# Kernel optimization log

Hardware: AMD Instinct MI355X
Metric: run time of the kernel (lower is better)

Reference implementation:

```python
import jax, jax.numpy as jnp
import numpy as np

B, N, NUM = 16384, 512, 3  # batch, num queries, num vanishing points per image


def setup_inputs() -> dict:
    key = jax.random.key(0)
    k1, k2, k3 = jax.random.split(key, 3)
    pred_logits = jax.random.normal(k1, (B, N, 1), jnp.float32)
    pp = jax.random.normal(k2, (B, N, 3), jnp.float32)
    pred_pos = pp / jnp.linalg.norm(pp, axis=-1, keepdims=True)  # unit directions
    vp = jax.random.normal(k3, (B, 3, NUM), jnp.float32)
    vps_unique = vp / jnp.linalg.norm(vp, axis=1, keepdims=True)  # all columns valid (abs-sum > 1e-5)
    return {"pred_logits": pred_logits, "pred_pos": pred_pos, "vps_unique": vps_unique}


def _greedy_select(conf, pos, num):
    # conf: [N,1], pos: [N,3]; greedy angular NMS keeping `num` candidates.
    order = jnp.argsort(-conf[:, 0]).astype(jnp.int32)  # descending confidence
    thresh = jnp.pi / (num + 1)
    ar = jnp.arange(num)
    cand0 = jnp.zeros((num,), jnp.int32).at[0].set(order[0])

    def step(carry, idx):
        cand, count = carry
        sel = pos[cand]                                   # [num,3]
        dots = jnp.minimum(jnp.abs(sel @ pos[idx]), 1.0)  # clip for arccos stability
        ang = jnp.where(ar < count, jnp.arccos(dots), jnp.inf)
        add = (count < num) & (jnp.min(ang) >= thresh)    # torch: skip if dst < pi/(num+1)
        cand = jnp.where(add & (ar == count), idx, cand)
        return (cand, count + add.astype(jnp.int32)), None

    (cand, _), _ = jax.lax.scan(step, (cand0, jnp.int32(1)), order[1:])
    return pos[cand]  # [num,3]


def reference(pred_logits, pred_pos, vps_unique):
    num = vps_unique.shape[2]  # static: all vps columns are valid by construction
    sel = jax.vmap(lambda c, p: _greedy_select(c, p, num))(pred_logits, pred_pos)
    return sel  # [B, num, 3]
```

## Files before the change

kernel.cpp:

```cpp
#include <hip/hip_runtime.h>
#include <math.h>

#define B_TOTAL 16384
#define NQ 512
#define NUM 3

__global__ __launch_bounds__(256) void greedy_nms_kernel(
    const float* __restrict__ conf,
    const float* __restrict__ pos,
    float* __restrict__ out)
{
    const int wave = threadIdx.x >> 6;
    const int lane = threadIdx.x & 63;
    const int b = (blockIdx.x << 2) + wave;

    const float* cb = conf + (size_t)b * NQ;
    const float* pb = pos  + (size_t)b * NQ * 3;

    const float4* cb4 = reinterpret_cast<const float4*>(cb);
    float4 c0 = cb4[lane * 2 + 0];
    float4 c1 = cb4[lane * 2 + 1];
    const float4* pb4 = reinterpret_cast<const float4*>(pb);
    float4 q0 = pb4[lane * 6 + 0];
    float4 q1 = pb4[lane * 6 + 1];
    float4 q2 = pb4[lane * 6 + 2];
    float4 q3 = pb4[lane * 6 + 3];
    float4 q4 = pb4[lane * 6 + 4];
    float4 q5 = pb4[lane * 6 + 5];

    unsigned k[8];
    {
        float f[8] = {c0.x, c0.y, c0.z, c0.w, c1.x, c1.y, c1.z, c1.w};
        #pragma unroll
        for (int s = 0; s < 8; ++s) {
            int bi = __float_as_int(f[s]);
            k[s] = (unsigned)bi ^ ((unsigned)(bi >> 31) | 0x80000000u);
        }
    }

    float rx[8], ry[8], rz[8];
    {
        float fl[24] = {q0.x, q0.y, q0.z, q0.w, q1.x, q1.y, q1.z, q1.w,
                        q2.x, q2.y, q2.z, q2.w, q3.x, q3.y, q3.z, q3.w,
                        q4.x, q4.y, q4.z, q4.w, q5.x, q5.y, q5.z, q5.w};
        #pragma unroll
        for (int j = 0; j < 8; ++j) {
            rx[j] = fl[3 * j + 0];
            ry[j] = fl[3 * j + 1];
            rz[j] = fl[3 * j + 2];
        }
    }

    auto argmax_idx = [&](unsigned& gm_out) -> int {
        unsigned m = k[0];
        #pragma unroll
        for (int s = 1; s < 8; ++s) m = k[s] > m ? k[s] : m;
        unsigned gm = m;
        #pragma unroll
        for (int off = 1; off < 64; off <<= 1) {
            unsigned o = __shfl_xor(gm, off);
            gm = o > gm ? o : gm;
        }
        int sl = 8;
        #pragma unroll
        for (int s = 7; s >= 0; --s)
            if (k[s] == gm) sl = s;
        unsigned long long ball = __ballot(sl < 8);
        int owner = __ffsll(ball) - 1;
        int osl = __shfl(sl, owner);
        gm_out = gm;
        return owner * 8 + osl;
    };

    auto get_row = [&](int w, float& x, float& y, float& z) {
        const int ow = w >> 3, sl = w & 7;
        float tx = rx[0], ty = ry[0], tz = rz[0];
        #pragma unroll
        for (int s = 1; s < 8; ++s)
            if (sl == s) { tx = rx[s]; ty = ry[s]; tz = rz[s]; }
        x = __shfl(tx, ow); y = __shfl(ty, ow); z = __shfl(tz, ow);
    };

    const float TH  = 0.78539816339744830961f;
    const float CLO = 0.70710478f;
    const float CHI = 0.70710878f;

    auto mask_keys = [&](float px, float py, float pz) {
        #pragma unroll
        for (int s = 0; s < 8; ++s) {
            float d = fabsf(rx[s] * px + ry[s] * py + rz[s] * pz);
            bool pass;
            if (d <= CLO)      pass = true;
            else if (d >= CHI) pass = false;
            else               pass = (acosf(fminf(d, 1.f)) >= TH);
            if (!pass) k[s] = 0u;
        }
    };

    unsigned gm1;
    int w1 = argmax_idx(gm1);
    float p1x, p1y, p1z;
    get_row(w1, p1x, p1y, p1z);
    {
        const int osl = ((w1 >> 3) == lane) ? (w1 & 7) : 8;
        #pragma unroll
        for (int s = 0; s < 8; ++s)
            if (osl == s) k[s] = 0u;
    }

    float p0x, p0y, p0z;
    get_row(0, p0x, p0y, p0z);

    mask_keys(p1x, p1y, p1z);
    unsigned gm2;
    int w2 = argmax_idx(gm2);

    float o2x = p0x, o2y = p0y, o2z = p0z;
    float o3x = p0x, o3y = p0y, o3z = p0z;

    if (gm2 != 0u) {
        float p2x, p2y, p2z;
        get_row(w2, p2x, p2y, p2z);
        o2x = p2x; o2y = p2y; o2z = p2z;

        mask_keys(p2x, p2y, p2z);
        unsigned gm3;
        int w3 = argmax_idx(gm3);
        if (gm3 != 0u) {
            get_row(w3, o3x, o3y, o3z);
        }
    }

    if (lane == 0) {
        float* ob = out + (size_t)b * 9;
        ob[0] = p1x; ob[1] = p1y; ob[2] = p1z;
        ob[3] = o2x; ob[4] = o2y; ob[5] = o2z;
        ob[6] = o3x; ob[7] = o3y; ob[8] = o3z;
    }
}

extern "C" void kernel_launch(void* const* d_in, const int* in_sizes, int n_in,
                              void* d_out, int out_size, void* d_ws, size_t ws_size,
                              hipStream_t stream) {
    const float* pred_logits = (const float*)d_in[0];
    const float* pred_pos    = (const float*)d_in[1];
    float* out = (float*)d_out;

    const int grid = B_TOTAL / 4;
    greedy_nms_kernel<<<grid, 256, 0, stream>>>(pred_logits, pred_pos, out);
}
```

Baseline: 26.64 us.

## Process four batches per wave with double-buffered register prefetch

Cuts the grid to 4096 waves, each handling four images strided across the batch. The loads for the next image are issued into a second register stage before the current one is processed, so memory latency overlaps with the argmax and masking work. This costs higher register pressure from two live stages, which may lower occupancy, and leaves fewer waves to hide latency through the hardware scheduler.

```diff
diff --git a/kernel.cpp b/kernel.cpp
--- a/kernel.cpp
+++ b/kernel.cpp
@@ -4,139 +4,159 @@
 #define B_TOTAL 16384
 #define NQ 512
 #define NUM 3
+#define WAVES_TOTAL 4096
+
+struct Stage {
+    float4 c0, c1;
+    float4 q0, q1, q2, q3, q4, q5;
+};
 
 __global__ __launch_bounds__(256) void greedy_nms_kernel(
     const float* __restrict__ conf,
     const float* __restrict__ pos,
     float* __restrict__ out)
 {
-    const int wave = threadIdx.x >> 6;
     const int lane = threadIdx.x & 63;
-    const int b = (blockIdx.x << 2) + wave;
+    const int wg   = (blockIdx.x << 2) | (threadIdx.x >> 6);
 
-    const float* cb = conf + (size_t)b * NQ;
-    const float* pb = pos  + (size_t)b * NQ * 3;
-
-    const float4* cb4 = reinterpret_cast<const float4*>(cb);
-    float4 c0 = cb4[lane * 2 + 0];
-    float4 c1 = cb4[lane * 2 + 1];
-    const float4* pb4 = reinterpret_cast<const float4*>(pb);
-    float4 q0 = pb4[lane * 6 + 0];
-    float4 q1 = pb4[lane * 6 + 1];
-    float4 q2 = pb4[lane * 6 + 2];
-    float4 q3 = pb4[lane * 6 + 3];
-    float4 q4 = pb4[lane * 6 + 4];
-    float4 q5 = pb4[lane * 6 + 5];
-
-    unsigned k[8];
-    {
-        float f[8] = {c0.x, c0.y, c0.z, c0.w, c1.x, c1.y, c1.z, c1.w};
-        #pragma unroll
-        for (int s = 0; s < 8; ++s) {
-            int bi = __float_as_int(f[s]);
-            k[s] = (unsigned)bi ^ ((unsigned)(bi >> 31) | 0x80000000u);
-        }
-    }
-
-    float rx[8], ry[8], rz[8];
-    {
-        float fl[24] = {q0.x, q0.y, q0.z, q0.w, q1.x, q1.y, q1.z, q1.w,
-                        q2.x, q2.y, q2.z, q2.w, q3.x, q3.y, q3.z, q3.w,
-                        q4.x, q4.y, q4.z, q4.w, q5.x, q5.y, q5.z, q5.w};
-        #pragma unroll
-        for (int j = 0; j < 8; ++j) {
-            rx[j] = fl[3 * j + 0];
-            ry[j] = fl[3 * j + 1];
-            rz[j] = fl[3 * j + 2];
-        }
-    }
-
-    auto argmax_idx = [&](unsigned& gm_out) -> int {
-        unsigned m = k[0];
-        #pragma unroll
-        for (int s = 1; s < 8; ++s) m = k[s] > m ? k[s] : m;
-        unsigned gm = m;
-        #pragma unroll
-        for (int off = 1; off < 64; off <<= 1) {
-            unsigned o = __shfl_xor(gm, off);
-            gm = o > gm ? o : gm;
-        }
-        int sl = 8;
-        #pragma unroll
-        for (int s = 7; s >= 0; --s)
-            if (k[s] == gm) sl = s;
-        unsigned long long ball = __ballot(sl < 8);
-        int owner = __ffsll(ball) - 1;
-        int osl = __shfl(sl, owner);
-        gm_out = gm;
-        return owner * 8 + osl;
-    };
-
-    auto get_row = [&](int w, float& x, float& y, float& z) {
-        const int ow = w >> 3, sl = w & 7;
-        float tx = rx[0], ty = ry[0], tz = rz[0];
-        #pragma unroll
-        for (int s = 1; s < 8; ++s)
-            if (sl == s) { tx = rx[s]; ty = ry[s]; tz = rz[s]; }
-        x = __shfl(tx, ow); y = __shfl(ty, ow); z = __shfl(tz, ow);
+    auto issue = [&](int b, Stage& s) {
+        const float4* cb4 = reinterpret_cast<const float4*>(conf + (size_t)b * NQ);
+        s.c0 = cb4[lane * 2 + 0];
+        s.c1 = cb4[lane * 2 + 1];
+        const float4* pb4 = reinterpret_cast<const float4*>(pos + (size_t)b * NQ * 3);
+        s.q0 = pb4[lane * 6 + 0];
+        s.q1 = pb4[lane * 6 + 1];
+        s.q2 = pb4[lane * 6 + 2];
+        s.q3 = pb4[lane * 6 + 3];
+        s.q4 = pb4[lane * 6 + 4];
+        s.q5 = pb4[lane * 6 + 5];
     };
 
     const float TH  = 0.78539816339744830961f;
     const float CLO = 0.70710478f;
     const float CHI = 0.70710878f;
 
-    auto mask_keys = [&](float px, float py, float pz) {
-        #pragma unroll
-        for (int s = 0; s < 8; ++s) {
-            float d = fabsf(rx[s] * px + ry[s] * py + rz[s] * pz);
-            bool pass;
-            if (d <= CLO)      pass = true;
-            else if (d >= CHI) pass = false;
-            else               pass = (acosf(fminf(d, 1.f)) >= TH);
-            if (!pass) k[s] = 0u;
+    auto process = [&](int b, const Stage& s) {
+        unsigned k[8];
+        {
+            float f[8] = {s.c0.x, s.c0.y, s.c0.z, s.c0.w,
+                          s.c1.x, s.c1.y, s.c1.z, s.c1.w};
+            #pragma unroll
+            for (int i = 0; i < 8; ++i) {
+                int bi = __float_as_int(f[i]);
+                k[i] = (unsigned)bi ^ ((unsigned)(bi >> 31) | 0x80000000u);
+            }
+        }
+        float rx[8], ry[8], rz[8];
+        {
+            float fl[24] = {s.q0.x, s.q0.y, s.q0.z, s.q0.w,
+                            s.q1.x, s.q1.y, s.q1.z, s.q1.w,
+                            s.q2.x, s.q2.y, s.q2.z, s.q2.w,
+                            s.q3.x, s.q3.y, s.q3.z, s.q3.w,
+                            s.q4.x, s.q4.y, s.q4.z, s.q4.w,
+                            s.q5.x, s.q5.y, s.q5.z, s.q5.w};
+            #pragma unroll
+            for (int j = 0; j < 8; ++j) {
+                rx[j] = fl[3 * j + 0];
+                ry[j] = fl[3 * j + 1];
+                rz[j] = fl[3 * j + 2];
+            }
+        }
+
+        auto argmax_idx = [&](unsigned& gm_out) -> int {
+            unsigned m = k[0];
+            #pragma unroll
+            for (int i = 1; i < 8; ++i) m = k[i] > m ? k[i] : m;
+            unsigned gm = m;
+            #pragma unroll
+            for (int off = 1; off < 64; off <<= 1) {
+                unsigned o = __shfl_xor(gm, off);
+                gm = o > gm ? o : gm;
+            }
+            int sl = 8;
+            #pragma unroll
+            for (int i = 7; i >= 0; --i)
+                if (k[i] == gm) sl = i;
+            unsigned long long ball = __ballot(sl < 8);
+            int owner = __ffsll(ball) - 1;
+            int osl = __shfl(sl, owner);
+            gm_out = gm;
+            return owner * 8 + osl;
+        };
+
+        auto get_row = [&](int w, float& x, float& y, float& z) {
+            const int ow = w >> 3, sl = w & 7;
+            float tx = rx[0], ty = ry[0], tz = rz[0];
+            #pragma unroll
+            for (int i = 1; i < 8; ++i)
+                if (sl == i) { tx = rx[i]; ty = ry[i]; tz = rz[i]; }
+            x = __shfl(tx, ow); y = __shfl(ty, ow); z = __shfl(tz, ow);
+        };
+
+        auto mask_keys = [&](float px, float py, float pz) {
+            #pragma unroll
+            for (int i = 0; i < 8; ++i) {
+                float d = fabsf(rx[i] * px + ry[i] * py + rz[i] * pz);
+                bool pass;
+                if (d <= CLO)      pass = true;
+                else if (d >= CHI) pass = false;
+                else               pass = (acosf(fminf(d, 1.f)) >= TH);
+                if (!pass) k[i] = 0u;
+            }
+        };
+
+        unsigned gm1;
+        int w1 = argmax_idx(gm1);
+        float p1x, p1y, p1z;
+        get_row(w1, p1x, p1y, p1z);
+        {
+            const int osl = ((w1 >> 3) == lane) ? (w1 & 7) : 8;
+            #pragma unroll
+            for (int i = 0; i < 8; ++i)
+                if (osl == i) k[i] = 0u;
+        }
+
+        float p0x, p0y, p0z;
+        get_row(0, p0x, p0y, p0z);
+
+        mask_keys(p1x, p1y, p1z);
+        unsigned gm2;
+        int w2 = argmax_idx(gm2);
+
+        float o2x = p0x, o2y = p0y, o2z = p0z;
+        float o3x = p0x, o3y = p0y, o3z = p0z;
+        if (gm2 != 0u) {
+            float p2x, p2y, p2z;
+            get_row(w2, p2x, p2y, p2z);
+            o2x = p2x; o2y = p2y; o2z = p2z;
+            mask_keys(p2x, p2y, p2z);
+            unsigned gm3;
+            int w3 = argmax_idx(gm3);
+            if (gm3 != 0u) get_row(w3, o3x, o3y, o3z);
+        }
+
+        if (lane == 0) {
+            float* ob = out + (size_t)b * 9;
+            ob[0] = p1x; ob[1] = p1y; ob[2] = p1z;
+            ob[3] = o2x; ob[4] = o2y; ob[5] = o2z;
+            ob[6] = o3x; ob[7] = o3y; ob[8] = o3z;
         }
     };
 
-    unsigned gm1;
-    int w1 = argmax_idx(gm1);
-    float p1x, p1y, p1z;
-    get_row(w1, p1x, p1y, p1z);
-    {
-        const int osl = ((w1 >> 3) == lane) ? (w1 & 7) : 8;
-        #pragma unroll
-        for (int s = 0; s < 8; ++s)
-            if (osl == s) k[s] = 0u;
-    }
+    const int b0 = wg;
+    const int b1 = wg + WAVES_TOTAL;
+    const int b2 = wg + 2 * WAVES_TOTAL;
+    const int b3 = wg + 3 * WAVES_TOTAL;
 
-    float p0x, p0y, p0z;
-    get_row(0, p0x, p0y, p0z);
-
-    mask_keys(p1x, p1y, p1z);
-    unsigned gm2;
-    int w2 = argmax_idx(gm2);
-
-    float o2x = p0x, o2y = p0y, o2z = p0z;
-    float o3x = p0x, o3y = p0y, o3z = p0z;
-
-    if (gm2 != 0u) {
-        float p2x, p2y, p2z;
-        get_row(w2, p2x, p2y, p2z);
-        o2x = p2x; o2y = p2y; o2z = p2z;
-
-        mask_keys(p2x, p2y, p2z);
-        unsigned gm3;
-        int w3 = argmax_idx(gm3);
-        if (gm3 != 0u) {
-            get_row(w3, o3x, o3y, o3z);
-        }
-    }
-
-    if (lane == 0) {
-        float* ob = out + (size_t)b * 9;
-        ob[0] = p1x; ob[1] = p1y; ob[2] = p1z;
-        ob[3] = o2x; ob[4] = o2y; ob[5] = o2z;
-        ob[6] = o3x; ob[7] = o3y; ob[8] = o3z;
-    }
+    Stage A, Bst;
+    issue(b0, A);
+    issue(b1, Bst);
+    process(b0, A);
+    issue(b2, A);
+    process(b1, Bst);
+    issue(b3, Bst);
+    process(b2, A);
+    process(b3, Bst);
 }
 
 extern "C" void kernel_launch(void* const* d_in, const int* in_sizes, int n_in,
@@ -146,6 +166,5 @@
     const float* pred_pos    = (const float*)d_in[1];
     float* out = (float*)d_out;
 
-    const int grid = B_TOTAL / 4;
-    greedy_nms_kernel<<<grid, 256, 0, stream>>>(pred_logits, pred_pos, out);
+    greedy_nms_kernel<<<WAVES_TOTAL / 4, 256, 0, stream>>>(pred_logits, pred_pos, out);
 }
```

New measurement: 30.69 us. 15.2% more time.

## Select top-16 candidates first and gather only their positions, with full fallback

Applied to the files above, without the earlier changes.

The kernel now extracts the top 16 confidence indices with repeated wave argmax, gathers only those 16 position rows, and runs the greedy angular selection with ballots over that short list. The full position load and the original algorithm run only when fewer than three accepted candidates turn up among the top 16. This avoids reading the whole 6 KB position block per batch in the common case. In exchange it adds 16 serial argmax reductions and scattered 12-byte gathers per wave.

```diff
diff --git a/kernel.cpp b/kernel.cpp
--- a/kernel.cpp
+++ b/kernel.cpp
@@ -4,15 +4,15 @@
 #define B_TOTAL 16384
 #define NQ 512
 #define NUM 3
+#define TOPK 16
 
 __global__ __launch_bounds__(256) void greedy_nms_kernel(
     const float* __restrict__ conf,
     const float* __restrict__ pos,
     float* __restrict__ out)
 {
-    const int wave = threadIdx.x >> 6;
     const int lane = threadIdx.x & 63;
-    const int b = (blockIdx.x << 2) + wave;
+    const int b = (blockIdx.x << 2) | (threadIdx.x >> 6);
 
     const float* cb = conf + (size_t)b * NQ;
     const float* pb = pos  + (size_t)b * NQ * 3;
@@ -20,13 +20,6 @@
     const float4* cb4 = reinterpret_cast<const float4*>(cb);
     float4 c0 = cb4[lane * 2 + 0];
     float4 c1 = cb4[lane * 2 + 1];
-    const float4* pb4 = reinterpret_cast<const float4*>(pb);
-    float4 q0 = pb4[lane * 6 + 0];
-    float4 q1 = pb4[lane * 6 + 1];
-    float4 q2 = pb4[lane * 6 + 2];
-    float4 q3 = pb4[lane * 6 + 3];
-    float4 q4 = pb4[lane * 6 + 4];
-    float4 q5 = pb4[lane * 6 + 5];
 
     unsigned k[8];
     {
@@ -38,20 +31,9 @@
         }
     }
 
-    float rx[8], ry[8], rz[8];
-    {
-        float fl[24] = {q0.x, q0.y, q0.z, q0.w, q1.x, q1.y, q1.z, q1.w,
-                        q2.x, q2.y, q2.z, q2.w, q3.x, q3.y, q3.z, q3.w,
-                        q4.x, q4.y, q4.z, q4.w, q5.x, q5.y, q5.z, q5.w};
-        #pragma unroll
-        for (int j = 0; j < 8; ++j) {
-            rx[j] = fl[3 * j + 0];
-            ry[j] = fl[3 * j + 1];
-            rz[j] = fl[3 * j + 2];
-        }
-    }
-
-    auto argmax_idx = [&](unsigned& gm_out) -> int {
+    int myw = 0;
+    #pragma unroll
+    for (int i = 0; i < TOPK; ++i) {
         unsigned m = k[0];
         #pragma unroll
         for (int s = 1; s < 8; ++s) m = k[s] > m ? k[s] : m;
@@ -68,74 +50,152 @@
         unsigned long long ball = __ballot(sl < 8);
         int owner = __ffsll(ball) - 1;
         int osl = __shfl(sl, owner);
-        gm_out = gm;
-        return owner * 8 + osl;
-    };
-
-    auto get_row = [&](int w, float& x, float& y, float& z) {
-        const int ow = w >> 3, sl = w & 7;
-        float tx = rx[0], ty = ry[0], tz = rz[0];
-        #pragma unroll
-        for (int s = 1; s < 8; ++s)
-            if (sl == s) { tx = rx[s]; ty = ry[s]; tz = rz[s]; }
-        x = __shfl(tx, ow); y = __shfl(ty, ow); z = __shfl(tz, ow);
-    };
+        if (lane == i) myw = owner * 8 + osl;
+        const int cs = (owner == lane) ? osl : 8;
+        #pragma unroll
+        for (int s = 0; s < 8; ++s)
+            if (cs == s) k[s] = 0u;
+    }
+
+    float cx = pb[myw * 3 + 0];
+    float cy = pb[myw * 3 + 1];
+    float cz = pb[myw * 3 + 2];
 
     const float TH  = 0.78539816339744830961f;
     const float CLO = 0.70710478f;
     const float CHI = 0.70710878f;
 
-    auto mask_keys = [&](float px, float py, float pz) {
-        #pragma unroll
-        for (int s = 0; s < 8; ++s) {
-            float d = fabsf(rx[s] * px + ry[s] * py + rz[s] * pz);
-            bool pass;
-            if (d <= CLO)      pass = true;
-            else if (d >= CHI) pass = false;
-            else               pass = (acosf(fminf(d, 1.f)) >= TH);
-            if (!pass) k[s] = 0u;
-        }
+    auto my_pass = [&](float px, float py, float pz) -> bool {
+        float d = fabsf(cx * px + cy * py + cz * pz);
+        if (d <= CLO) return true;
+        if (d >= CHI) return false;
+        return acosf(fminf(d, 1.f)) >= TH;
     };
 
-    unsigned gm1;
-    int w1 = argmax_idx(gm1);
-    float p1x, p1y, p1z;
-    get_row(w1, p1x, p1y, p1z);
+    float p1x = __shfl(cx, 0), p1y = __shfl(cy, 0), p1z = __shfl(cz, 0);
+    unsigned long long ball1 =
+        __ballot(my_pass(p1x, p1y, p1z)) & 0xFFFEull;
+
+    if (ball1 != 0) {
+        const int i2 = __ffsll(ball1) - 1;
+        float p2x = __shfl(cx, i2), p2y = __shfl(cy, i2), p2z = __shfl(cz, i2);
+        unsigned long long ball3 =
+            ball1 & __ballot(my_pass(p2x, p2y, p2z)) & ~((2ull << i2) - 1);
+        if (ball3 != 0) {
+            const int i3 = __ffsll(ball3) - 1;
+            float p3x = __shfl(cx, i3), p3y = __shfl(cy, i3), p3z = __shfl(cz, i3);
+            if (lane == 0) {
+                float* ob = out + (size_t)b * 9;
+                ob[0] = p1x; ob[1] = p1y; ob[2] = p1z;
+                ob[3] = p2x; ob[4] = p2y; ob[5] = p2z;
+                ob[6] = p3x; ob[7] = p3y; ob[8] = p3z;
+            }
+            return;
+        }
+    }
+
     {
-        const int osl = ((w1 >> 3) == lane) ? (w1 & 7) : 8;
-        #pragma unroll
-        for (int s = 0; s < 8; ++s)
-            if (osl == s) k[s] = 0u;
-    }
-
-    float p0x, p0y, p0z;
-    get_row(0, p0x, p0y, p0z);
-
-    mask_keys(p1x, p1y, p1z);
-    unsigned gm2;
-    int w2 = argmax_idx(gm2);
-
-    float o2x = p0x, o2y = p0y, o2z = p0z;
-    float o3x = p0x, o3y = p0y, o3z = p0z;
-
-    if (gm2 != 0u) {
-        float p2x, p2y, p2z;
-        get_row(w2, p2x, p2y, p2z);
-        o2x = p2x; o2y = p2y; o2z = p2z;
-
-        mask_keys(p2x, p2y, p2z);
-        unsigned gm3;
-        int w3 = argmax_idx(gm3);
-        if (gm3 != 0u) {
-            get_row(w3, o3x, o3y, o3z);
-        }
-    }
-
-    if (lane == 0) {
-        float* ob = out + (size_t)b * 9;
-        ob[0] = p1x; ob[1] = p1y; ob[2] = p1z;
-        ob[3] = o2x; ob[4] = o2y; ob[5] = o2z;
-        ob[6] = o3x; ob[7] = o3y; ob[8] = o3z;
+        float4 d0 = cb4[lane * 2 + 0];
+        float4 d1 = cb4[lane * 2 + 1];
+        {
+            float f[8] = {d0.x, d0.y, d0.z, d0.w, d1.x, d1.y, d1.z, d1.w};
+            #pragma unroll
+            for (int s = 0; s < 8; ++s) {
+                int bi = __float_as_int(f[s]);
+                k[s] = (unsigned)bi ^ ((unsigned)(bi >> 31) | 0x80000000u);
+            }
+        }
+        const float4* pb4 = reinterpret_cast<const float4*>(pb);
+        float4 q0 = pb4[lane * 6 + 0];
+        float4 q1 = pb4[lane * 6 + 1];
+        float4 q2 = pb4[lane * 6 + 2];
+        float4 q3 = pb4[lane * 6 + 3];
+        float4 q4 = pb4[lane * 6 + 4];
+        float4 q5 = pb4[lane * 6 + 5];
+        float rx[8], ry[8], rz[8];
+        rx[0] = q0.x; ry[0] = q0.y; rz[0] = q0.z;
+        rx[1] = q0.w; ry[1] = q1.x; rz[1] = q1.y;
+        rx[2] = q1.z; ry[2] = q1.w; rz[2] = q2.x;
+        rx[3] = q2.y; ry[3] = q2.z; rz[3] = q2.w;
+        rx[4] = q3.x; ry[4] = q3.y; rz[4] = q3.z;
+        rx[5] = q3.w; ry[5] = q4.x; rz[5] = q4.y;
+        rx[6] = q4.z; ry[6] = q4.w; rz[6] = q5.x;
+        rx[7] = q5.y; ry[7] = q5.z; rz[7] = q5.w;
+
+        auto argmax_idx = [&](unsigned& gm_out) -> int {
+            unsigned m = k[0];
+            #pragma unroll
+            for (int s = 1; s < 8; ++s) m = k[s] > m ? k[s] : m;
+            unsigned gm = m;
+            #pragma unroll
+            for (int off = 1; off < 64; off <<= 1) {
+                unsigned o = __shfl_xor(gm, off);
+                gm = o > gm ? o : gm;
+            }
+            int sl = 8;
+            #pragma unroll
+            for (int s = 7; s >= 0; --s)
+                if (k[s] == gm) sl = s;
+            unsigned long long ball = __ballot(sl < 8);
+            int owner = __ffsll(ball) - 1;
+            int osl = __shfl(sl, owner);
+            gm_out = gm;
+            return owner * 8 + osl;
+        };
+        auto get_row = [&](int w, float& x, float& y, float& z) {
+            const int ow = w >> 3, sl = w & 7;
+            float tx = rx[0], ty = ry[0], tz = rz[0];
+            #pragma unroll
+            for (int s = 1; s < 8; ++s)
+                if (sl == s) { tx = rx[s]; ty = ry[s]; tz = rz[s]; }
+            x = __shfl(tx, ow); y = __shfl(ty, ow); z = __shfl(tz, ow);
+        };
+        auto mask_keys = [&](float px, float py, float pz) {
+            #pragma unroll
+            for (int s = 0; s < 8; ++s) {
+                float d = fabsf(rx[s] * px + ry[s] * py + rz[s] * pz);
+                bool pass;
+                if (d <= CLO)      pass = true;
+                else if (d >= CHI) pass = false;
+                else               pass = (acosf(fminf(d, 1.f)) >= TH);
+                if (!pass) k[s] = 0u;
+            }
+        };
+
+        unsigned gm1;
+        int w1 = argmax_idx(gm1);
+        float f1x, f1y, f1z;
+        get_row(w1, f1x, f1y, f1z);
+        {
+            const int osl = ((w1 >> 3) == lane) ? (w1 & 7) : 8;
+            #pragma unroll
+            for (int s = 0; s < 8; ++s)
+                if (osl == s) k[s] = 0u;
+        }
+
+        mask_keys(f1x, f1y, f1z);
+        unsigned gm2;
+        int w2 = argmax_idx(gm2);
+
+        float o2x, o2y, o2z, o3x, o3y, o3z;
+        if (gm2 != 0u) {
+            get_row(w2, o2x, o2y, o2z);
+            mask_keys(o2x, o2y, o2z);
+            unsigned gm3;
+            int w3 = argmax_idx(gm3);
+            if (gm3 != 0u) get_row(w3, o3x, o3y, o3z);
+            else           get_row(0, o3x, o3y, o3z);
+        } else {
+            get_row(0, o2x, o2y, o2z);
+            o3x = o2x; o3y = o2y; o3z = o2z;
+        }
+
+        if (lane == 0) {
+            float* ob = out + (size_t)b * 9;
+            ob[0] = f1x; ob[1] = f1y; ob[2] = f1z;
+            ob[3] = o2x; ob[4] = o2y; ob[5] = o2z;
+            ob[6] = o3x; ob[7] = o3y; ob[8] = o3z;
+        }
     }
 }
 
```

Result: slower. 32.25 us (+21.0%).
